# Kernel optimization log

Hardware: AMD Instinct MI355X
Metric: run time of the kernel (lower is better)

Reference implementation:

```python
import jax, jax.numpy as jnp
import numpy as np

B, C, H, W = 4, 128, 64, 64
NUM_HEADS = 4
HEAD_DIM = C // NUM_HEADS


def setup_inputs() -> dict:
    key = jax.random.key(0)
    ks = jax.random.split(key, 9)
    s = 0.02
    return {
        "x": jax.random.normal(ks[0], (B, C, H, W), dtype=jnp.float32),
        "wq": jax.random.normal(ks[1], (C, C), dtype=jnp.float32) * s,
        "bq": jax.random.normal(ks[2], (C,), dtype=jnp.float32) * s,
        "wk": jax.random.normal(ks[3], (C, C), dtype=jnp.float32) * s,
        "bk": jax.random.normal(ks[4], (C,), dtype=jnp.float32) * s,
        "wv": jax.random.normal(ks[5], (C, C), dtype=jnp.float32) * s,
        "bv": jax.random.normal(ks[6], (C,), dtype=jnp.float32) * s,
        "wo": jax.random.normal(ks[7], (C, C), dtype=jnp.float32) * s,
        "bo": jax.random.normal(ks[8], (C,), dtype=jnp.float32) * s,
    }


def _proj(w, b, xf):
    # 1x1 conv == channel-mixing linear: xf is (B, C, N)
    return jnp.einsum("oc,bcn->bon", w, xf) + b[None, :, None]


def reference(x, wq, bq, wk, bk, wv, bv, wo, bo):
    b, c, h, w = x.shape
    n = h * w
    nh, hd = NUM_HEADS, HEAD_DIM
    xf = x.reshape(b, c, n)
    q = _proj(wq, bq, xf).reshape(b, nh, hd, n)
    k = _proj(wk, bk, xf).reshape(b, nh, hd, n)
    v = _proj(wv, bv, xf).reshape(b, nh, hd, n)
    # scores: (b, heads, n, n)
    scores = jnp.einsum("bhdn,bhdm->bhnm", q, k) / jnp.sqrt(jnp.float32(hd)).astype(x.dtype)
    prob = jax.nn.softmax(scores, axis=-1)
    # attn_out: (b, heads, head_dim, n)
    attn = jnp.einsum("bhnm,bhdm->bhdn", prob, v).reshape(b, c, n)
    out = _proj(wo, bo, attn).reshape(b, c, h, w)
    return x + out
```

## Files before the change

kernel.cpp:

```cpp
#include <hip/hip_runtime.h>
#include <hip/hip_bf16.h>

#define BB 4
#define CC 128
#define NN 4096
#define NHEAD 4
#define HDIM 32
#define KSPLIT 4

typedef short bf16x8_t __attribute__((ext_vector_type(8)));
typedef float f32x4_t __attribute__((ext_vector_type(4)));
typedef int i32x4_t __attribute__((ext_vector_type(4)));

#define MFMA16(a, b, c) __builtin_amdgcn_mfma_f32_16x16x32_bf16(a, b, c, 0, 0, 0)
#define EXP2(x) __builtin_amdgcn_exp2f(x)

#define QSCALE (0.17677669529663687f * 1.4426950408889634f)

static __device__ inline unsigned short f2bf(float f) {
  unsigned u = __builtin_bit_cast(unsigned, f);
  u += 0x7fffu + ((u >> 16) & 1u);
  return (unsigned short)(u >> 16);
}
static __device__ inline unsigned pk2(float lo, float hi) {
  return (unsigned)f2bf(lo) | ((unsigned)f2bf(hi) << 16);
}
static __device__ inline unsigned pack_trunc(float lo, float hi) {
  return __builtin_amdgcn_perm(__builtin_bit_cast(unsigned, hi),
                               __builtin_bit_cast(unsigned, lo), 0x07060302u);
}
static __device__ inline float bfu_lo(unsigned v) {
  return __builtin_bit_cast(float, v << 16);
}
static __device__ inline float bfu_hi(unsigned v) {
  return __builtin_bit_cast(float, v & 0xFFFF0000u);
}

static __device__ inline bf16x8_t wfrag_f32(const float* __restrict__ Wp, float sc) {
  float4 a = *(const float4*)(Wp);
  float4 b = *(const float4*)(Wp + 4);
  i32x4_t pi = {(int)pk2(a.x * sc, a.y * sc), (int)pk2(a.z * sc, a.w * sc),
                (int)pk2(b.x * sc, b.y * sc), (int)pk2(b.z * sc, b.w * sc)};
  return __builtin_bit_cast(bf16x8_t, pi);
}

static __device__ inline void gload_lds16(const unsigned short* gsrc, void* ldst) {
  __builtin_amdgcn_global_load_lds(
      (const __attribute__((address_space(1))) unsigned int*)gsrc,
      (__attribute__((address_space(3))) unsigned int*)ldst, 16, 0, 0);
}

static __device__ inline void waitcnt_vm0() {
  asm volatile("s_waitcnt vmcnt(0)" ::: "memory");
}

__global__ __launch_bounds__(256) void qkv_mfma_kernel(
    const float* __restrict__ x,
    const float* __restrict__ wq, const float* __restrict__ wk,
    const float* __restrict__ wv,
    const float* __restrict__ bq, const float* __restrict__ bk,
    const float* __restrict__ bv,
    unsigned short* __restrict__ qt, unsigned short* __restrict__ kt,
    unsigned short* __restrict__ vg) {
  __shared__ __attribute__((aligned(16))) unsigned short xsb[64][136];
  __shared__ unsigned short vt[64][66];
  const int b = blockIdx.y, nt = blockIdx.x;
  const int proj = blockIdx.z >> 1, half = blockIdx.z & 1;
  const int tid = threadIdx.x;

#pragma unroll
  for (int i = 0; i < 8; i++) {
    int f = tid + 256 * i;
    int c = f >> 4, n4 = (f & 15) * 4;
    float4 v4 = *(const float4*)(x + ((size_t)b * CC + c) * NN + nt * 64 + n4);
    xsb[n4 + 0][c] = f2bf(v4.x);
    xsb[n4 + 1][c] = f2bf(v4.y);
    xsb[n4 + 2][c] = f2bf(v4.z);
    xsb[n4 + 3][c] = f2bf(v4.w);
  }
  __syncthreads();

  const int lane = tid & 63, w = tid >> 6;
  const int l16 = lane & 15, g = lane >> 4;
  const int nl = w * 16;
  const int ngl = nt * 64 + nl;

  bf16x8_t xf[4];
#pragma unroll
  for (int ks = 0; ks < 4; ks++)
    xf[ks] = *(const bf16x8_t*)&xsb[nl + l16][ks * 32 + g * 8];

  const float* wm = (proj == 0) ? wq : (proj == 1) ? wk : wv;
  const float* bias = (proj == 0) ? bq : (proj == 1) ? bk : bv;
  const float bsc = (proj == 0) ? QSCALE : 1.0f;
  unsigned short* qkdst = proj ? kt : qt;

#pragma unroll
  for (int i = 0; i < 4; i++) {
    const int ot = half * 4 + i;
    f32x4_t acc;
#pragma unroll
    for (int r = 0; r < 4; r++) acc[r] = bias[ot * 16 + g * 4 + r] * bsc;
#pragma unroll
    for (int ks = 0; ks < 4; ks++) {
      bf16x8_t wf = wfrag_f32(wm + (size_t)(ot * 16 + l16) * CC + ks * 32 + g * 8, bsc);
      acc = MFMA16(wf, xf[ks], acc);
    }
    if (proj < 2) {
      unsigned p0 = pk2(acc[0], acc[1]);
      unsigned p1 = pk2(acc[2], acc[3]);
      unsigned q0 = (unsigned)__shfl_xor((int)p0, 16);
      unsigned q1 = (unsigned)__shfl_xor((int)p1, 16);
      if ((g & 1) == 0) {
        int hh = ot >> 1, dblk = (ot & 1) * 2 + (g >> 1);
        unsigned short* dst =
            qkdst + (((size_t)(b * NHEAD + hh) * 4 + dblk) * NN + ngl + l16) * 8;
        uint4 val = make_uint4(p0, p1, q0, q1);
        *(uint4*)dst = val;
      }
    } else {
#pragma unroll
      for (int r = 0; r < 4; r++) vt[i * 16 + g * 4 + r][nl + l16] = f2bf(acc[r]);
    }
  }

  if (proj == 2) {
    __syncthreads();
#pragma unroll
    for (int c = 0; c < 2; c++) {
      int cid = c * 256 + tid;
      int hh_l = cid >> 8, inner = cid & 255;
      int hh = half * 2 + hh_l;
      int g2 = inner & 3, l16v = (inner >> 2) & 15, fh = inner >> 6;
      int fv = fh >> 1, halfv = fh & 1;
      int o_l = hh_l * 32 + halfv * 16 + l16v;
      int n0 = fv * 32 + g2 * 4;
      unsigned d0 = *(const unsigned*)&vt[o_l][n0];
      unsigned d1 = *(const unsigned*)&vt[o_l][n0 + 2];
      unsigned d2 = *(const unsigned*)&vt[o_l][n0 + 16];
      unsigned d3 = *(const unsigned*)&vt[o_l][n0 + 18];
      uint4 val = make_uint4(d0, d1, d2, d3);
      *(uint4*)(vg + (((size_t)(b * NHEAD + hh) * 64 + nt) * 256 + inner) * 8) = val;
    }
  }
}

__global__ __launch_bounds__(256, 4) void attn_mfma7_kernel(
    const unsigned short* __restrict__ qt, const unsigned short* __restrict__ kt,
    const unsigned short* __restrict__ vg,
    unsigned* __restrict__ obf, float* __restrict__ lpart) {
  __shared__ __attribute__((aligned(16))) unsigned short smem[2][4096];

  const int chunk = blockIdx.x & (KSPLIT - 1), nt = blockIdx.x / KSPLIT;
  const int h = blockIdx.y, b = blockIdx.z;
  const int bh = b * NHEAD + h;
  const int tid = threadIdx.x, lane = tid & 63, wid = tid >> 6;
  const int l16 = lane & 15, g = lane >> 4;
  const int nbase = nt * 128 + wid * 32;

  const unsigned short* qb = qt + (size_t)bh * NN * HDIM;
  const unsigned short* kb = kt + (size_t)bh * NN * HDIM;
  const unsigned short* vgb = vg + (size_t)bh * 64 * 2048;

  const bf16x8_t qf0 = *(const bf16x8_t*)(qb + ((size_t)g * NN + nbase + l16) * 8);
  const bf16x8_t qf1 = *(const bf16x8_t*)(qb + ((size_t)g * NN + nbase + 16 + l16) * 8);

  f32x4_t o00 = {0, 0, 0, 0}, o01 = {0, 0, 0, 0};
  f32x4_t o10 = {0, 0, 0, 0}, o11 = {0, 0, 0, 0};
  f32x4_t la = {0, 0, 0, 0}, lb = {0, 0, 0, 0};
  const f32x4_t zf = {0, 0, 0, 0};
  const i32x4_t onesi = {0x3F803F80, 0x3F803F80, 0x3F803F80, 0x3F803F80};
  const bf16x8_t ones = __builtin_bit_cast(bf16x8_t, onesi);

  const int NITER = 64 / KSPLIT;
  const int mt0 = chunk * NITER;

  const unsigned short* ksrc = kb + ((size_t)g * NN + mt0 * 64 + wid * 16 + l16) * 8;
  const unsigned short* vsrc = vgb + (size_t)mt0 * 2048 + (size_t)((wid * 16 + l16) * 4 + g) * 8;

  auto stage = [&](int p, int i) {
    gload_lds16(ksrc + (size_t)i * 512, &smem[p][wid * 512]);
    gload_lds16(vsrc + (size_t)i * 2048, &smem[p][2048 + wid * 512]);
  };

  auto body = [&](int p) {
    const unsigned short* sk = &smem[p][0];
    bf16x8_t k0 = *(const bf16x8_t*)(sk + 0 * 512 + lane * 8);
    bf16x8_t k1 = *(const bf16x8_t*)(sk + 1 * 512 + lane * 8);
    bf16x8_t k2 = *(const bf16x8_t*)(sk + 2 * 512 + lane * 8);
    bf16x8_t k3 = *(const bf16x8_t*)(sk + 3 * 512 + lane * 8);
    bf16x8_t vf0 = *(const bf16x8_t*)(sk + 2048 + 0 * 512 + lane * 8);
    bf16x8_t vf2 = *(const bf16x8_t*)(sk + 2048 + 1 * 512 + lane * 8);
    bf16x8_t vf1 = *(const bf16x8_t*)(sk + 2048 + 2 * 512 + lane * 8);
    bf16x8_t vf3 = *(const bf16x8_t*)(sk + 2048 + 3 * 512 + lane * 8);

    f32x4_t sA0 = MFMA16(k0, qf0, zf), sA1 = MFMA16(k1, qf0, zf);
    f32x4_t sA2 = MFMA16(k2, qf0, zf), sA3 = MFMA16(k3, qf0, zf);
    f32x4_t sB0 = MFMA16(k0, qf1, zf), sB1 = MFMA16(k1, qf1, zf);
    f32x4_t sB2 = MFMA16(k2, qf1, zf), sB3 = MFMA16(k3, qf1, zf);

#pragma unroll
    for (int r = 0; r < 4; r++) {
      sA0[r] = EXP2(sA0[r]); sA1[r] = EXP2(sA1[r]);
      sA2[r] = EXP2(sA2[r]); sA3[r] = EXP2(sA3[r]);
      sB0[r] = EXP2(sB0[r]); sB1[r] = EXP2(sB1[r]);
      sB2[r] = EXP2(sB2[r]); sB3[r] = EXP2(sB3[r]);
    }

    i32x4_t pA0i = {(int)pack_trunc(sA0[0], sA0[1]), (int)pack_trunc(sA0[2], sA0[3]),
                    (int)pack_trunc(sA1[0], sA1[1]), (int)pack_trunc(sA1[2], sA1[3])};
    i32x4_t pA1i = {(int)pack_trunc(sA2[0], sA2[1]), (int)pack_trunc(sA2[2], sA2[3]),
                    (int)pack_trunc(sA3[0], sA3[1]), (int)pack_trunc(sA3[2], sA3[3])};
    i32x4_t pB0i = {(int)pack_trunc(sB0[0], sB0[1]), (int)pack_trunc(sB0[2], sB0[3]),
                    (int)pack_trunc(sB1[0], sB1[1]), (int)pack_trunc(sB1[2], sB1[3])};
    i32x4_t pB1i = {(int)pack_trunc(sB2[0], sB2[1]), (int)pack_trunc(sB2[2], sB2[3]),
                    (int)pack_trunc(sB3[0], sB3[1]), (int)pack_trunc(sB3[2], sB3[3])};
    bf16x8_t pA0 = __builtin_bit_cast(bf16x8_t, pA0i);
    bf16x8_t pA1 = __builtin_bit_cast(bf16x8_t, pA1i);
    bf16x8_t pB0 = __builtin_bit_cast(bf16x8_t, pB0i);
    bf16x8_t pB1 = __builtin_bit_cast(bf16x8_t, pB1i);

    o00 = MFMA16(vf0, pA0, o00); o00 = MFMA16(vf1, pA1, o00);
    o01 = MFMA16(vf2, pA0, o01); o01 = MFMA16(vf3, pA1, o01);
    o10 = MFMA16(vf0, pB0, o10); o10 = MFMA16(vf1, pB1, o10);
    o11 = MFMA16(vf2, pB0, o11); o11 = MFMA16(vf3, pB1, o11);

    la = MFMA16(ones, pA0, la); la = MFMA16(ones, pA1, la);
    lb = MFMA16(ones, pB0, lb); lb = MFMA16(ones, pB1, lb);
  };

  stage(0, 0);
  waitcnt_vm0();
  __syncthreads();
  for (int mi = 0; mi < NITER; mi += 2) {
    stage(1, mi + 1);
    body(0);
    waitcnt_vm0();
    __syncthreads();
    if (mi + 2 < NITER) stage(0, mi + 2);
    body(1);
    waitcnt_vm0();
    __syncthreads();
  }

  unsigned* ob = obf + (size_t)(chunk * BB * NHEAD + bh) * 32 * 2048;
  const int dw = (nbase >> 1) + l16;
#pragma unroll
  for (int r = 0; r < 4; r++) {
    ob[(size_t)(g * 4 + r) * 2048 + dw] = pk2(o00[r], o10[r]);
    ob[(size_t)(16 + g * 4 + r) * 2048 + dw] = pk2(o01[r], o11[r]);
  }
  if (g == 0) {
    float* lb_ = lpart + (size_t)(chunk * BB * NHEAD + bh) * NN;
    lb_[nbase + l16] = la[0];
    lb_[nbase + 16 + l16] = lb[0];
  }
}

__global__ __launch_bounds__(256) void outc_kernel(
    const unsigned* __restrict__ obf, const float* __restrict__ lpart,
    const float* __restrict__ wo, const float* __restrict__ bo,
    const float* __restrict__ x, float* __restrict__ out) {
  __shared__ __attribute__((aligned(16))) unsigned short asb[32][136];
  const int b = blockIdx.y, nt2 = blockIdx.x;
  const int nb = nt2 * 32, dwb = nt2 * 16;
  const int tid = threadIdx.x, lane = tid & 63;
  const int wv = tid >> 6, l16 = lane & 15, g = lane >> 4;

  {
    float l0 = 0.f, l1 = 0.f;
#pragma unroll
    for (int c = 0; c < KSPLIT; c++) {
      const float* lp = lpart + (size_t)(c * BB * NHEAD + b * NHEAD + wv) * NN + nb;
      l0 += lp[l16];
      l1 += lp[16 + l16];
    }
    float inv0 = 1.f / l0, inv1 = 1.f / l1;
#pragma unroll
    for (int j = 0; j < 8; j++) {
      int d = g * 8 + j;
      float s0 = 0.f, s1 = 0.f;
#pragma unroll
      for (int c = 0; c < KSPLIT; c++) {
        unsigned v = obf[(size_t)(c * BB * NHEAD + b * NHEAD + wv) * 65536 +
                         (size_t)d * 2048 + dwb + l16];
        s0 += bfu_lo(v);
        s1 += bfu_hi(v);
      }
      int cfull = wv * 32 + d;
      asb[l16][cfull] = f2bf(s0 * inv0);
      asb[16 + l16][cfull] = f2bf(s1 * inv1);
    }
  }
  __syncthreads();

#pragma unroll
  for (int oi = 0; oi < 2; oi++) {
    const int ot = wv * 2 + oi;
    f32x4_t a0, a1;
#pragma unroll
    for (int r = 0; r < 4; r++) { a0[r] = bo[ot * 16 + g * 4 + r]; a1[r] = a0[r]; }
#pragma unroll
    for (int ks = 0; ks < 4; ks++) {
      bf16x8_t af = wfrag_f32(wo + (size_t)(ot * 16 + l16) * CC + ks * 32 + g * 8, 1.0f);
      bf16x8_t b0 = *(const bf16x8_t*)&asb[l16][ks * 32 + g * 8];
      bf16x8_t b1 = *(const bf16x8_t*)&asb[16 + l16][ks * 32 + g * 8];
      a0 = MFMA16(af, b0, a0);
      a1 = MFMA16(af, b1, a1);
    }
#pragma unroll
    for (int r = 0; r < 4; r++) {
      int o = ot * 16 + g * 4 + r;
      size_t ad = ((size_t)b * CC + o) * NN + nb + l16;
      out[ad] = a0[r] + x[ad];
      out[ad + 16] = a1[r] + x[ad + 16];
    }
  }
}

extern "C" void kernel_launch(void* const* d_in, const int* in_sizes, int n_in,
                              void* d_out, int out_size, void* d_ws, size_t ws_size,
                              hipStream_t stream) {
  const float* x  = (const float*)d_in[0];
  const float* wq = (const float*)d_in[1];
  const float* bq = (const float*)d_in[2];
  const float* wk = (const float*)d_in[3];
  const float* bk = (const float*)d_in[4];
  const float* wv = (const float*)d_in[5];
  const float* bv = (const float*)d_in[6];
  const float* wo = (const float*)d_in[7];
  const float* bo = (const float*)d_in[8];
  float* out = (float*)d_out;

  char* w = (char*)d_ws;
  const size_t SZ = (size_t)BB * NHEAD * NN * HDIM * 2;
  unsigned short* qt = (unsigned short*)w;
  unsigned short* kt = (unsigned short*)(w + SZ);
  unsigned short* vg = (unsigned short*)(w + 2 * SZ);
  unsigned* obf = (unsigned*)(w + 3 * SZ);
  float* lpart = (float*)(w + 3 * SZ +
                          (size_t)KSPLIT * BB * NHEAD * HDIM * NN * 2);

  qkv_mfma_kernel<<<dim3(NN / 64, BB, 6), 256, 0, stream>>>(
      x, wq, wk, wv, bq, bk, bv, qt, kt, vg);
  attn_mfma7_kernel<<<dim3((NN / 128) * KSPLIT, NHEAD, BB), 256, 0, stream>>>(
      qt, kt, vg, obf, lpart);
  outc_kernel<<<dim3(NN / 32, BB), 256, 0, stream>>>(obf, lpart, wo, bo, x, out);
}
```

Baseline: 149.4 us.

## Replace bf16 MFMA projections with fp32 FMA tiled GEMMs in QKV and output kernels

Rewrites the QKV projection and output projection kernels to use plain fp32 FMA loops over LDS-tiled inputs and weights, instead of bf16 MFMA with on-the-fly weight conversion. The aim looks like better accuracy (no bf16 rounding of x and weights before the projections) and removal of the per-lane weight conversion cost. In exchange the projections run on scalar FP32 ALUs rather than matrix cores, which costs far more instructions. The output kernel also adds extra LDS staging of wo per 32-row tile, with a barrier before each of those tiles.

```diff
diff --git a/kernel.cpp b/kernel.cpp
--- a/kernel.cpp
+++ b/kernel.cpp
@@ -36,14 +36,6 @@
   return __builtin_bit_cast(float, v & 0xFFFF0000u);
 }
 
-static __device__ inline bf16x8_t wfrag_f32(const float* __restrict__ Wp, float sc) {
-  float4 a = *(const float4*)(Wp);
-  float4 b = *(const float4*)(Wp + 4);
-  i32x4_t pi = {(int)pk2(a.x * sc, a.y * sc), (int)pk2(a.z * sc, a.w * sc),
-                (int)pk2(b.x * sc, b.y * sc), (int)pk2(b.z * sc, b.w * sc)};
-  return __builtin_bit_cast(bf16x8_t, pi);
-}
-
 static __device__ inline void gload_lds16(const unsigned short* gsrc, void* ldst) {
   __builtin_amdgcn_global_load_lds(
       (const __attribute__((address_space(1))) unsigned int*)gsrc,
@@ -54,7 +46,7 @@
   asm volatile("s_waitcnt vmcnt(0)" ::: "memory");
 }
 
-__global__ __launch_bounds__(256) void qkv_mfma_kernel(
+__global__ __launch_bounds__(256) void qkv_fp32_kernel(
     const float* __restrict__ x,
     const float* __restrict__ wq, const float* __restrict__ wk,
     const float* __restrict__ wv,
@@ -62,85 +54,91 @@
     const float* __restrict__ bv,
     unsigned short* __restrict__ qt, unsigned short* __restrict__ kt,
     unsigned short* __restrict__ vg) {
-  __shared__ __attribute__((aligned(16))) unsigned short xsb[64][136];
-  __shared__ unsigned short vt[64][66];
-  const int b = blockIdx.y, nt = blockIdx.x;
-  const int proj = blockIdx.z >> 1, half = blockIdx.z & 1;
+  __shared__ float xs[32][132];
+  __shared__ float wsm[32][33];
+  const int z = blockIdx.z;
+  const int proj = z >> 2, b = z & 3;
+  const int otile = blockIdx.y, ntile = blockIdx.x;
+  const float* Wm = (proj == 0) ? wq : (proj == 1) ? wk : wv;
+  const float* bias = (proj == 0) ? bq : (proj == 1) ? bk : bv;
+  const float* src = x + (size_t)b * CC * NN;
   const int tid = threadIdx.x;
-
-#pragma unroll
-  for (int i = 0; i < 8; i++) {
-    int f = tid + 256 * i;
-    int c = f >> 4, n4 = (f & 15) * 4;
-    float4 v4 = *(const float4*)(x + ((size_t)b * CC + c) * NN + nt * 64 + n4);
-    xsb[n4 + 0][c] = f2bf(v4.x);
-    xsb[n4 + 1][c] = f2bf(v4.y);
-    xsb[n4 + 2][c] = f2bf(v4.z);
-    xsb[n4 + 3][c] = f2bf(v4.w);
+  const int o_loc = tid >> 3;
+  const int lane8 = tid & 7;
+
+  float4 acc[4];
+  {
+    float bo = bias[otile * 32 + o_loc];
+    for (int i = 0; i < 4; i++) acc[i] = make_float4(bo, bo, bo, bo);
+  }
+
+  for (int cc = 0; cc < 4; cc++) {
+    for (int i = 0; i < 4; i++) {
+      int f = tid + 256 * i;
+      int c = f >> 5;
+      int col4 = f & 31;
+      float4 xx = *(const float4*)(src + (size_t)(cc * 32 + c) * NN + ntile * 128 + col4 * 4);
+      *(float4*)&xs[c][col4 * 4] = xx;
+    }
+    {
+      int o_w = tid >> 3, c4 = tid & 7;
+      float4 wv4 = *(const float4*)(Wm + (size_t)(otile * 32 + o_w) * CC + cc * 32 + c4 * 4);
+      wsm[o_w][c4 * 4 + 0] = wv4.x;
+      wsm[o_w][c4 * 4 + 1] = wv4.y;
+      wsm[o_w][c4 * 4 + 2] = wv4.z;
+      wsm[o_w][c4 * 4 + 3] = wv4.w;
+    }
+    __syncthreads();
+    for (int c = 0; c < 32; c++) {
+      float wv_ = wsm[o_loc][c];
+      for (int i = 0; i < 4; i++) {
+        float4 xx = *(const float4*)&xs[c][lane8 * 4 + 32 * i];
+        acc[i].x += wv_ * xx.x;
+        acc[i].y += wv_ * xx.y;
+        acc[i].z += wv_ * xx.z;
+        acc[i].w += wv_ * xx.w;
+      }
+    }
+    __syncthreads();
+  }
+
+  const float bsc = (proj == 0) ? QSCALE : 1.0f;
+  for (int i = 0; i < 4; i++) {
+    float4 a = acc[i];
+    a.x *= bsc; a.y *= bsc; a.z *= bsc; a.w *= bsc;
+    *(float4*)&xs[o_loc][lane8 * 4 + 32 * i] = a;
   }
   __syncthreads();
 
-  const int lane = tid & 63, w = tid >> 6;
-  const int l16 = lane & 15, g = lane >> 4;
-  const int nl = w * 16;
-  const int ngl = nt * 64 + nl;
-
-  bf16x8_t xf[4];
-#pragma unroll
-  for (int ks = 0; ks < 4; ks++)
-    xf[ks] = *(const bf16x8_t*)&xsb[nl + l16][ks * 32 + g * 8];
-
-  const float* wm = (proj == 0) ? wq : (proj == 1) ? wk : wv;
-  const float* bias = (proj == 0) ? bq : (proj == 1) ? bk : bv;
-  const float bsc = (proj == 0) ? QSCALE : 1.0f;
-  unsigned short* qkdst = proj ? kt : qt;
-
-#pragma unroll
-  for (int i = 0; i < 4; i++) {
-    const int ot = half * 4 + i;
-    f32x4_t acc;
-#pragma unroll
-    for (int r = 0; r < 4; r++) acc[r] = bias[ot * 16 + g * 4 + r] * bsc;
-#pragma unroll
-    for (int ks = 0; ks < 4; ks++) {
-      bf16x8_t wf = wfrag_f32(wm + (size_t)(ot * 16 + l16) * CC + ks * 32 + g * 8, bsc);
-      acc = MFMA16(wf, xf[ks], acc);
-    }
-    if (proj < 2) {
-      unsigned p0 = pk2(acc[0], acc[1]);
-      unsigned p1 = pk2(acc[2], acc[3]);
-      unsigned q0 = (unsigned)__shfl_xor((int)p0, 16);
-      unsigned q1 = (unsigned)__shfl_xor((int)p1, 16);
-      if ((g & 1) == 0) {
-        int hh = ot >> 1, dblk = (ot & 1) * 2 + (g >> 1);
-        unsigned short* dst =
-            qkdst + (((size_t)(b * NHEAD + hh) * 4 + dblk) * NN + ngl + l16) * 8;
-        uint4 val = make_uint4(p0, p1, q0, q1);
-        *(uint4*)dst = val;
-      }
-    } else {
-#pragma unroll
-      for (int r = 0; r < 4; r++) vt[i * 16 + g * 4 + r][nl + l16] = f2bf(acc[r]);
-    }
-  }
-
-  if (proj == 2) {
-    __syncthreads();
-#pragma unroll
-    for (int c = 0; c < 2; c++) {
-      int cid = c * 256 + tid;
-      int hh_l = cid >> 8, inner = cid & 255;
-      int hh = half * 2 + hh_l;
+  if (proj < 2) {
+    unsigned short* dst = proj ? kt : qt;
+#pragma unroll
+    for (int c2 = 0; c2 < 2; c2++) {
+      int u = tid + 256 * c2;
+      int dblk = u >> 7, n_loc = u & 127;
+      unsigned w0 = pk2(xs[dblk * 8 + 0][n_loc], xs[dblk * 8 + 1][n_loc]);
+      unsigned w1 = pk2(xs[dblk * 8 + 2][n_loc], xs[dblk * 8 + 3][n_loc]);
+      unsigned w2 = pk2(xs[dblk * 8 + 4][n_loc], xs[dblk * 8 + 5][n_loc]);
+      unsigned w3 = pk2(xs[dblk * 8 + 6][n_loc], xs[dblk * 8 + 7][n_loc]);
+      uint4 val = make_uint4(w0, w1, w2, w3);
+      *(uint4*)(dst + (((size_t)(b * NHEAD + otile) * 4 + dblk) * NN + ntile * 128 + n_loc) * 8) = val;
+    }
+  } else {
+#pragma unroll
+    for (int c2 = 0; c2 < 2; c2++) {
+      int u = tid + 256 * c2;
+      int mt_loc = u >> 8, inner = u & 255;
       int g2 = inner & 3, l16v = (inner >> 2) & 15, fh = inner >> 6;
-      int fv = fh >> 1, halfv = fh & 1;
-      int o_l = hh_l * 32 + halfv * 16 + l16v;
-      int n0 = fv * 32 + g2 * 4;
-      unsigned d0 = *(const unsigned*)&vt[o_l][n0];
-      unsigned d1 = *(const unsigned*)&vt[o_l][n0 + 2];
-      unsigned d2 = *(const unsigned*)&vt[o_l][n0 + 16];
-      unsigned d3 = *(const unsigned*)&vt[o_l][n0 + 18];
-      uint4 val = make_uint4(d0, d1, d2, d3);
-      *(uint4*)(vg + (((size_t)(b * NHEAD + hh) * 64 + nt) * 256 + inner) * 8) = val;
+      int fv = fh >> 1, half = fh & 1;
+      int d = half * 16 + l16v;
+      int nb2 = mt_loc * 64 + fv * 32 + g2 * 4;
+      unsigned w0 = pk2(xs[d][nb2 + 0], xs[d][nb2 + 1]);
+      unsigned w1 = pk2(xs[d][nb2 + 2], xs[d][nb2 + 3]);
+      unsigned w2 = pk2(xs[d][nb2 + 16], xs[d][nb2 + 17]);
+      unsigned w3 = pk2(xs[d][nb2 + 18], xs[d][nb2 + 19]);
+      uint4 val = make_uint4(w0, w1, w2, w3);
+      int mt = ntile * 2 + mt_loc;
+      *(uint4*)(vg + (((size_t)(b * NHEAD + otile) * 64 + mt) * 256 + inner) * 8) = val;
     }
   }
 }
@@ -261,17 +259,18 @@
     const unsigned* __restrict__ obf, const float* __restrict__ lpart,
     const float* __restrict__ wo, const float* __restrict__ bo,
     const float* __restrict__ x, float* __restrict__ out) {
-  __shared__ __attribute__((aligned(16))) unsigned short asb[32][136];
+  __shared__ float as[128][33];
+  __shared__ float wsm[32][129];
   const int b = blockIdx.y, nt2 = blockIdx.x;
   const int nb = nt2 * 32, dwb = nt2 * 16;
   const int tid = threadIdx.x, lane = tid & 63;
-  const int wv = tid >> 6, l16 = lane & 15, g = lane >> 4;
+  const int hw = tid >> 6, l16 = lane & 15, g = lane >> 4;
 
   {
     float l0 = 0.f, l1 = 0.f;
 #pragma unroll
     for (int c = 0; c < KSPLIT; c++) {
-      const float* lp = lpart + (size_t)(c * BB * NHEAD + b * NHEAD + wv) * NN + nb;
+      const float* lp = lpart + (size_t)(c * BB * NHEAD + b * NHEAD + hw) * NN + nb;
       l0 += lp[l16];
       l1 += lp[16 + l16];
     }
@@ -282,39 +281,50 @@
       float s0 = 0.f, s1 = 0.f;
 #pragma unroll
       for (int c = 0; c < KSPLIT; c++) {
-        unsigned v = obf[(size_t)(c * BB * NHEAD + b * NHEAD + wv) * 65536 +
+        unsigned v = obf[(size_t)(c * BB * NHEAD + b * NHEAD + hw) * 65536 +
                          (size_t)d * 2048 + dwb + l16];
         s0 += bfu_lo(v);
         s1 += bfu_hi(v);
       }
-      int cfull = wv * 32 + d;
-      asb[l16][cfull] = f2bf(s0 * inv0);
-      asb[16 + l16][cfull] = f2bf(s1 * inv1);
-    }
-  }
-  __syncthreads();
-
-#pragma unroll
-  for (int oi = 0; oi < 2; oi++) {
-    const int ot = wv * 2 + oi;
-    f32x4_t a0, a1;
-#pragma unroll
-    for (int r = 0; r < 4; r++) { a0[r] = bo[ot * 16 + g * 4 + r]; a1[r] = a0[r]; }
-#pragma unroll
-    for (int ks = 0; ks < 4; ks++) {
-      bf16x8_t af = wfrag_f32(wo + (size_t)(ot * 16 + l16) * CC + ks * 32 + g * 8, 1.0f);
-      bf16x8_t b0 = *(const bf16x8_t*)&asb[l16][ks * 32 + g * 8];
-      bf16x8_t b1 = *(const bf16x8_t*)&asb[16 + l16][ks * 32 + g * 8];
-      a0 = MFMA16(af, b0, a0);
-      a1 = MFMA16(af, b1, a1);
-    }
-#pragma unroll
-    for (int r = 0; r < 4; r++) {
-      int o = ot * 16 + g * 4 + r;
-      size_t ad = ((size_t)b * CC + o) * NN + nb + l16;
-      out[ad] = a0[r] + x[ad];
-      out[ad + 16] = a1[r] + x[ad + 16];
-    }
+      int cfull = hw * 32 + d;
+      as[cfull][l16] = s0 * inv0;
+      as[cfull][16 + l16] = s1 * inv1;
+    }
+  }
+
+  const int o_loc = tid >> 3, lane8 = tid & 7;
+#pragma unroll
+  for (int ot4 = 0; ot4 < 4; ot4++) {
+#pragma unroll
+    for (int i = 0; i < 4; i++) {
+      int f = tid + 256 * i;
+      int o_w = f >> 5, c4 = f & 31;
+      float4 wv4 = *(const float4*)(wo + (size_t)(ot4 * 32 + o_w) * CC + c4 * 4);
+      *(float4*)&wsm[o_w][c4 * 4] = wv4;
+    }
+    __syncthreads();
+
+    float4 a;
+    {
+      float bv_ = bo[ot4 * 32 + o_loc];
+      a = make_float4(bv_, bv_, bv_, bv_);
+    }
+    for (int c = 0; c < CC; c++) {
+      float wv_ = wsm[o_loc][c];
+      float4 xx = *(const float4*)&as[c][lane8 * 4];
+      a.x += wv_ * xx.x;
+      a.y += wv_ * xx.y;
+      a.z += wv_ * xx.z;
+      a.w += wv_ * xx.w;
+    }
+    {
+      int o = ot4 * 32 + o_loc;
+      size_t ad = ((size_t)b * CC + o) * NN + nb + lane8 * 4;
+      float4 xv = *(const float4*)(x + ad);
+      a.x += xv.x; a.y += xv.y; a.z += xv.z; a.w += xv.w;
+      *(float4*)(out + ad) = a;
+    }
+    __syncthreads();
   }
 }
 
@@ -341,7 +351,7 @@
   float* lpart = (float*)(w + 3 * SZ +
                           (size_t)KSPLIT * BB * NHEAD * HDIM * NN * 2);
 
-  qkv_mfma_kernel<<<dim3(NN / 64, BB, 6), 256, 0, stream>>>(
+  qkv_fp32_kernel<<<dim3(NN / 128, CC / 32, 12), 256, 0, stream>>>(
       x, wq, wk, wv, bq, bk, bv, qt, kt, vg);
   attn_mfma7_kernel<<<dim3((NN / 128) * KSPLIT, NHEAD, BB), 256, 0, stream>>>(
       qt, kt, vg, obf, lpart);
```

New measurement: 172.4 us. 15.4% more time.
